# Performance work log

Hardware: AMD Instinct MI355X
Metric: run time of the kernel (lower is better)

Reference implementation:

```python
import jax, jax.numpy as jnp
import numpy as np
import math

B, T, D = 4, 4096, 256


def setup_inputs() -> dict:
    key = jax.random.key(0)
    ks = jax.random.split(key, 12)
    stdv = 1.0 / math.sqrt(D)
    u = lambda k, shape, s: jax.random.uniform(k, shape, jnp.float32, -s, s)
    return {
        "query": jax.random.normal(ks[0], (B, T, D), jnp.float32),
        "value": jax.random.normal(ks[1], (B, T, D), jnp.float32),
        # gate vectors, init uniform(-1/sqrt(D), 1/sqrt(D)) per reset_parameters
        "q_vec": u(ks[2], (D,), stdv),
        "k_vec": u(ks[3], (D,), stdv),
        "v_vec": u(ks[4], (D,), stdv),
        # nn.Linear params (torch default init: uniform(-1/sqrt(fan_in), ...))
        "Wq": u(ks[5], (D, D), stdv), "bq": u(ks[6], (D,), stdv),
        "Ws": u(ks[7], (D, D), stdv), "bs": u(ks[8], (D,), stdv),
        "Wt": u(ks[9], (D, D), stdv), "bt": u(ks[10], (D,), stdv),
    }


def reference(query, value, q_vec, k_vec, v_vec, Wq, bq, Ws, bs, Wt, bt):
    d = query.shape[-1]
    # q = Linear(query) * sigmoid(query_vector)
    q = (jnp.einsum('btd,ed->bte', query, Wq) + bq) * jax.nn.sigmoid(q_vec)
    # k = value * sigmoid(key_vector)
    k = value * jax.nn.sigmoid(k_vec)
    # v gate: infer=False branch -> GLU-style gate of sigmoid(value_vector)
    vv = jax.nn.sigmoid(v_vec)
    v_gate = jax.nn.sigmoid(Ws @ vv + bs) * jnp.tanh(Wt @ vv + bt)
    v = value * v_gate
    # scores [B, T, T]
    w = jnp.einsum('bqd,bkd->bqk', q, k) / jnp.sqrt(jnp.float32(d))
    # causal: multiply by tril mask then replace exact zeros with -inf
    # (faithful to the original's weight[weight==0]=-inf quirk)
    Tn = w.shape[-1]
    tril = jnp.tril(jnp.ones((Tn, Tn), w.dtype))
    w = w * tril
    w = jnp.where(w == 0.0, -jnp.inf, w)
    attn = jax.nn.softmax(w, axis=-1)
    return jnp.einsum('bqk,bkd->bqd', attn, v)
```

## Files before the change

kernel.cpp:

```cpp
#include <hip/hip_runtime.h>
#include <math.h>

#define D 256
#define T 4096
#define KT (17408/2)
#define VT (20480/2)
#define PSTR ((size_t)4*T*D)

typedef __attribute__((ext_vector_type(8))) short bf16x8;
typedef __attribute__((ext_vector_type(4))) float f32x4;
typedef __attribute__((ext_vector_type(4))) unsigned short u16x4;

__device__ __forceinline__ unsigned short f2bf(float x){
  unsigned int u = __float_as_uint(x);
  unsigned int r = (u + 0x7FFFu + ((u >> 16) & 1u)) >> 16;
  return (unsigned short)r;
}
__device__ __forceinline__ float bf2f(unsigned short h){
  return __uint_as_float(((unsigned int)h) << 16);
}

__device__ __forceinline__ void gl_lds16(const void* g, void* l){
  __builtin_amdgcn_global_load_lds((const __attribute__((address_space(1))) unsigned int*)g,
                                   (__attribute__((address_space(3))) unsigned int*)l, 16, 0, 0);
}

__global__ __launch_bounds__(256) void prep_kernel(
    const float* __restrict__ q_vec, const float* __restrict__ k_vec,
    const float* __restrict__ v_vec, const float* __restrict__ Ws,
    const float* __restrict__ bs, const float* __restrict__ Wt,
    const float* __restrict__ bt, const float* __restrict__ Wq,
    float* __restrict__ gates, unsigned short* __restrict__ wq_g){
  int t = threadIdx.x;
  if(blockIdx.x == 0){
    __shared__ float vv[D];
    vv[t]         = 1.f/(1.f + __expf(-v_vec[t]));
    gates[t]      = 1.f/(1.f + __expf(-q_vec[t]));
    gates[D + t]  = 1.f/(1.f + __expf(-k_vec[t]));
    __syncthreads();
    const f32x4* wsr = (const f32x4*)(Ws + (size_t)t*D);
    const f32x4* wtr = (const f32x4*)(Wt + (size_t)t*D);
    const f32x4* vvv = (const f32x4*)vv;
    f32x4 a0 = {0,0,0,0}, a1 = {0,0,0,0}, c0 = {0,0,0,0}, c1 = {0,0,0,0};
    for(int i=0;i<64;i+=2){
      f32x4 v0 = vvv[i], v1 = vvv[i+1];
      a0 += wsr[i]*v0; a1 += wsr[i+1]*v1;
      c0 += wtr[i]*v0; c1 += wtr[i+1]*v1;
    }
    f32x4 as = a0 + a1, cs = c0 + c1;
    float s1 = bs[t] + as[0]+as[1]+as[2]+as[3];
    float s2 = bt[t] + cs[0]+cs[1]+cs[2]+cs[3];
    gates[2*D + t] = (1.f/(1.f + __expf(-s1))) * tanhf(s2);
  } else {
    int kc = blockIdx.x - 1;
    const float* src = Wq + (size_t)t*D + kc*32;
    unsigned short* dst = wq_g + (size_t)kc*10240 + t*40;
    #pragma unroll
    for(int u=0;u<4;u++){
      bf16x8 pk;
      #pragma unroll
      for(int x=0;x<8;x++) pk[x] = (short)f2bf(src[u*8+x]);
      *(bf16x8*)&dst[u*8] = pk;
    }
  }
}

__global__ __launch_bounds__(256) void mid_kernel(
    const float* __restrict__ query, const unsigned short* __restrict__ wq_g,
    const float* __restrict__ bq, const float* __restrict__ gates,
    unsigned short* __restrict__ q_g,
    const float* __restrict__ value,
    unsigned short* __restrict__ k_g, unsigned short* __restrict__ vt_g){
  __shared__ __align__(16) unsigned short smem[2][10240];
  int tid = threadIdx.x;
  if(blockIdx.x < 256){
    int w = tid >> 6; int l = tid & 63;
    int lr = l & 15, lc = l >> 4;
    int r0 = blockIdx.x * 64;
    f32x4 acc[16];
    #pragma unroll
    for(int n=0;n<16;n++) acc[n] = (f32x4){0.f,0.f,0.f,0.f};
    const float* qrow = query + (size_t)(r0 + w*16 + lr)*D;
    #pragma unroll
    for(int i=0;i<5;i++){ int c = i*256 + tid; gl_lds16(wq_g + c*8, (char*)smem[0] + c*16); }
    __syncthreads();
    int cur = 0;
    for(int kc=0; kc<8; kc++){
      if(kc < 7){
        #pragma unroll
        for(int i=0;i<5;i++){ int c = i*256 + tid;
          gl_lds16(wq_g + (size_t)(kc+1)*10240 + c*8, (char*)smem[cur^1] + c*16); }
      }
      bf16x8 af;
      {
        const float* s = qrow + kc*32 + lc*8;
        #pragma unroll
        for(int x=0;x<8;x++) af[x] = (short)f2bf(s[x]);
      }
      #pragma unroll
      for(int n=0;n<16;n++){
        bf16x8 bfrag = *(const bf16x8*)&smem[cur][(n*16 + lr)*40 + lc*8];
        acc[n] = __builtin_amdgcn_mfma_f32_16x16x32_bf16(af, bfrag, acc[n], 0, 0, 0);
      }
      __syncthreads();
      cur ^= 1;
    }
    #pragma unroll
    for(int n=0;n<16;n++){
      int col = n*16 + lr;
      float bb = bq[col], gg = gates[col];
      #pragma unroll
      for(int r=0;r<4;r++){
        int row = r0 + w*16 + lc*4 + r;
        q_g[(size_t)row*D + col] = f2bf((acc[n][r] + bb) * gg);
      }
    }
  } else {
    int bid2 = blockIdx.x - 256;
    int b = bid2 >> 7, jt = bid2 & 127;
    const float* vbase = value + ((size_t)b*T + jt*32)*D;
    const float* gk = gates + D;
    const float* vg = gates + 2*D;
    unsigned short* kt = k_g  + (size_t)bid2 * KT;
    unsigned short* vt = vt_g + (size_t)bid2 * VT;
    #pragma unroll
    for(int i=0;i<4;i++){
      int g = i*256 + tid; int j = g >> 5, c = g & 31;
      const float* src = vbase + j*D + c*8;
      bf16x8 pk;
      #pragma unroll
      for(int x=0;x<8;x++) pk[x] = (short)f2bf(src[x] * gk[c*8+x]);
      *(bf16x8*)&kt[j*264 + c*8] = pk;
    }
    float* lds = (float*)smem;
    for(int c=0;c<4;c++){
      __syncthreads();
      {
        int row = tid >> 3, cg = tid & 7;
        const float* src = vbase + (size_t)row*D + c*64 + cg*8;
        f32x4 v0 = *(const f32x4*)src;
        f32x4 v1 = *(const f32x4*)(src + 4);
        *(f32x4*)&lds[row*68 + cg*8]     = v0;
        *(f32x4*)&lds[row*68 + cg*8 + 4] = v1;
      }
      __syncthreads();
      {
        int d0l = tid >> 2, u = tid & 3;
        int d0 = c*64 + d0l;
        float gd = vg[d0];
        bf16x8 pk;
        #pragma unroll
        for(int x=0;x<8;x++){
          int p = u*8 + x;
          int ksrc = ((p>>3)<<2) + (p&3) + (((p>>2)&1)<<4);
          pk[x] = (short)f2bf(lds[ksrc*68 + d0l] * gd);
        }
        *(bf16x8*)&vt[d0*40 + u*8] = pk;
      }
    }
  }
}

__global__ __launch_bounds__(512, 4) void flash_kernel(
    const unsigned short* __restrict__ q_g,
    const unsigned short* __restrict__ k_g,
    const unsigned short* __restrict__ vt_g,
    unsigned short* __restrict__ parts,
    float* __restrict__ ml, int logS){
  __shared__ __align__(16) unsigned short kbuf[2][KT];
  __shared__ __align__(16) unsigned short vbuf[2][VT];
  int tid = threadIdx.x; int w = tid >> 6, l = tid & 63;
  int lr = l & 15, lc = l >> 4;
  int S = 1 << logS;
  int bid = blockIdx.x;
  int x = bid & 7; int b = x >> 1; int p = x & 1;
  int item = bid >> 3;
  int half = S >> 1;
  int rblk = 31 - (item / half);
  int s = p*half + (item & (half - 1));
  int r0 = rblk * 128;
  int wrow0 = r0 + w*16;
  int nt = 4*rblk + 4;
  int jt0 = (s*nt) >> logS, jt1 = ((s+1)*nt) >> logS;
  int gr = wrow0 + lr;

  bf16x8 qf[8];
  {
    const unsigned short* qbase = q_g + ((size_t)b*T + wrow0 + lr)*D + lc*8;
    #pragma unroll
    for(int kc=0;kc<8;kc++) qf[kc] = *(const bf16x8*)(qbase + kc*32);
  }
  f32x4 o[16];
  #pragma unroll
  for(int n=0;n<16;n++) o[n] = (f32x4){0.f,0.f,0.f,0.f};
  float m = -INFINITY, lsum = 0.f;

  const unsigned short* ktb = k_g  + (size_t)b*128*KT;
  const unsigned short* vtb = vt_g + (size_t)b*128*VT;

  if(jt1 > jt0){
    const unsigned short* ks = ktb + (size_t)jt0*KT;
    const unsigned short* vs = vtb + (size_t)jt0*VT;
    for(int c=w; c<37; c+=8){
      if(c < 17) gl_lds16(ks + c*512 + l*8, (char*)kbuf[jt0&1] + c*1024);
      else       gl_lds16(vs + (c-17)*512 + l*8, (char*)vbuf[jt0&1] + (c-17)*1024);
    }
  }

  for(int jt=jt0; jt<jt1; jt++){
    int cur = jt & 1;
    asm volatile("s_waitcnt vmcnt(0)" ::: "memory");
    __builtin_amdgcn_s_barrier();
    __builtin_amdgcn_sched_barrier(0);
    if(jt+1 < jt1){
      const unsigned short* ks = ktb + (size_t)(jt+1)*KT;
      const unsigned short* vs = vtb + (size_t)(jt+1)*VT;
      for(int c=w; c<37; c+=8){
        if(c < 17) gl_lds16(ks + c*512 + l*8, (char*)kbuf[cur^1] + c*1024);
        else       gl_lds16(vs + (c-17)*512 + l*8, (char*)vbuf[cur^1] + (c-17)*1024);
      }
    }
    int j0 = jt*32;
    bool active = (j0 <= wrow0 + 15);
    if(active){
      f32x4 s0a = {0,0,0,0}, s0b = {0,0,0,0}, s1a = {0,0,0,0}, s1b = {0,0,0,0};
      #pragma unroll
      for(int kc=0;kc<4;kc++){
        bf16x8 k0 = *(const bf16x8*)&kbuf[cur][lr*264        + (kc*4 + lc)*8];
        bf16x8 k1 = *(const bf16x8*)&kbuf[cur][(16 + lr)*264 + (kc*4 + lc)*8];
        bf16x8 k0h = *(const bf16x8*)&kbuf[cur][lr*264        + ((kc+4)*4 + lc)*8];
        bf16x8 k1h = *(const bf16x8*)&kbuf[cur][(16 + lr)*264 + ((kc+4)*4 + lc)*8];
        s0a = __builtin_amdgcn_mfma_f32_16x16x32_bf16(k0,  qf[kc],   s0a, 0,0,0);
        s1a = __builtin_amdgcn_mfma_f32_16x16x32_bf16(k1,  qf[kc],   s1a, 0,0,0);
        s0b = __builtin_amdgcn_mfma_f32_16x16x32_bf16(k0h, qf[kc+4], s0b, 0,0,0);
        s1b = __builtin_amdgcn_mfma_f32_16x16x32_bf16(k1h, qf[kc+4], s1b, 0,0,0);
      }
      f32x4 s0 = s0a + s0b, s1 = s1a + s1b;
      float sv0[4], sv1[4];
      #pragma unroll
      for(int r=0;r<4;r++){
        float x0 = s0[r]*0.0625f; int gj0 = j0 + lc*4 + r;
        float x1 = s1[r]*0.0625f; int gj1 = gj0 + 16;
        if(gj0 > gr || x0 == 0.0f) x0 = -INFINITY;
        if(gj1 > gr || x1 == 0.0f) x1 = -INFINITY;
        sv0[r]=x0; sv1[r]=x1;
      }
      float pmax = fmaxf(fmaxf(fmaxf(sv0[0],sv0[1]),fmaxf(sv0[2],sv0[3])),
                         fmaxf(fmaxf(sv1[0],sv1[1]),fmaxf(sv1[2],sv1[3])));
      pmax = fmaxf(pmax, __shfl_xor(pmax, 16));
      pmax = fmaxf(pmax, __shfl_xor(pmax, 32));
      bool mv = (pmax > m + 8.0f);
      float mn = mv ? pmax : m;
      float alpha = mv ? __expf(m - mn) : 1.0f;
      float p0[4], p1[4];
      #pragma unroll
      for(int r=0;r<4;r++){
        p0[r] = (sv0[r] == -INFINITY) ? 0.f : __expf(sv0[r] - mn);
        p1[r] = (sv1[r] == -INFINITY) ? 0.f : __expf(sv1[r] - mn);
      }
      unsigned long long anymv = __builtin_amdgcn_ballot_w64(mv);
      if(anymv){
        float a0 = __shfl(alpha, lc*4 + 0);
        float a1 = __shfl(alpha, lc*4 + 1);
        float a2 = __shfl(alpha, lc*4 + 2);
        float a3 = __shfl(alpha, lc*4 + 3);
        #pragma unroll
        for(int n=0;n<16;n++){
          o[n][0] *= a0; o[n][1] *= a1; o[n][2] *= a2; o[n][3] *= a3;
        }
      }
      float ps = ((p0[0]+p0[1])+(p0[2]+p0[3])) + ((p1[0]+p1[1])+(p1[2]+p1[3]));
      lsum = lsum*alpha + ps;
      m = mn;
      bf16x8 pa;
      #pragma unroll
      for(int r=0;r<4;r++){ pa[r] = (short)f2bf(p0[r]); pa[4+r] = (short)f2bf(p1[r]); }
      #pragma unroll
      for(int n=0;n<16;n++){
        bf16x8 vf = *(const bf16x8*)&vbuf[cur][(n*16 + lr)*40 + lc*8];
        o[n] = __builtin_amdgcn_mfma_f32_16x16x32_bf16(pa, vf, o[n], 0,0,0);
      }
    }
  }

  unsigned short* obase = parts + (size_t)s*PSTR + ((size_t)b*T + wrow0)*D;
  #pragma unroll
  for(int r=0;r<4;r++){
    #pragma unroll
    for(int n=0;n<16;n++){
      obase[(size_t)(lc*4 + r)*D + n*16 + lr] = f2bf(o[n][r]);
    }
  }
  lsum += __shfl_xor(lsum, 16);
  lsum += __shfl_xor(lsum, 32);
  if(l < 16){
    float* mlb = ml + ((size_t)s*4*T + (size_t)b*T + wrow0 + lr)*2;
    mlb[0] = m; mlb[1] = lsum;
  }
}

__global__ __launch_bounds__(256) void combine_kernel(
    const unsigned short* __restrict__ parts, const float* __restrict__ ml,
    float* __restrict__ out, int S){
  size_t idx = (size_t)blockIdx.x*256 + threadIdx.x;
  size_t e = idx*4;
  size_t row = e >> 8;
  float msv[8], lsv[8];
  float mm = -INFINITY;
  for(int s=0;s<S;s++){
    msv[s] = ml[((size_t)s*4*T + row)*2];
    lsv[s] = ml[((size_t)s*4*T + row)*2 + 1];
    mm = fmaxf(mm, msv[s]);
  }
  float denom = 0.f;
  f32x4 acc = {0.f,0.f,0.f,0.f};
  for(int s=0;s<S;s++){
    float as = __expf(msv[s] - mm);
    if(as != 0.0f){
      denom += as*lsv[s];
      u16x4 v = *(const u16x4*)&parts[(size_t)s*PSTR + e];
      #pragma unroll
      for(int xx=0;xx<4;xx++) acc[xx] += as*bf2f(v[xx]);
    }
  }
  float inv = 1.0f/denom;
  f32x4 r;
  #pragma unroll
  for(int xx=0;xx<4;xx++) r[xx] = acc[xx]*inv;
  *(f32x4*)&out[e] = r;
}

extern "C" void kernel_launch(void* const* d_in, const int* in_sizes, int n_in,
                              void* d_out, int out_size, void* d_ws, size_t ws_size,
                              hipStream_t stream){
  (void)in_sizes; (void)n_in; (void)out_size;
  const float* query = (const float*)d_in[0];
  const float* value = (const float*)d_in[1];
  const float* q_vec = (const float*)d_in[2];
  const float* k_vec = (const float*)d_in[3];
  const float* v_vec = (const float*)d_in[4];
  const float* Wq    = (const float*)d_in[5];
  const float* bq    = (const float*)d_in[6];
  const float* Ws    = (const float*)d_in[7];
  const float* bs    = (const float*)d_in[8];
  const float* Wt    = (const float*)d_in[9];
  const float* bt    = (const float*)d_in[10];
  char* ws = (char*)d_ws;
  unsigned short* q_g  = (unsigned short*)(ws);
  unsigned short* k_g  = (unsigned short*)(ws + 8388608);
  unsigned short* vt_g = (unsigned short*)(ws + 17301504);
  unsigned short* wq_g = (unsigned short*)(ws + 27787264);
  float* gates         = (float*)(ws + 27951104);
  unsigned short* parts= (unsigned short*)(ws + 27955200);
  float* out = (float*)d_out;

  size_t base = 27955200;
  size_t mlsz = (size_t)8*4*T*2*4;
  int logS;
  if(ws_size >= base + 8*PSTR*2 + mlsz)      logS = 3;
  else if(ws_size >= base + 4*PSTR*2 + mlsz) logS = 2;
  else                                       logS = 1;
  int S = 1 << logS;
  float* ml = (float*)(ws + base + (size_t)S*PSTR*2);

  hipLaunchKernelGGL(prep_kernel, dim3(9),   dim3(256), 0, stream,
                     q_vec, k_vec, v_vec, Ws, bs, Wt, bt, Wq, gates, wq_g);
  hipLaunchKernelGGL(mid_kernel,  dim3(768), dim3(256), 0, stream,
                     query, wq_g, bq, gates, q_g, value, k_g, vt_g);
  hipLaunchKernelGGL(flash_kernel, dim3(128*S), dim3(512), 0, stream,
                     q_g, k_g, vt_g, parts, ml, logS);
  hipLaunchKernelGGL(combine_kernel, dim3((4*T*D/4)/256), dim3(256), 0, stream,
                     parts, ml, out, S);
}
```

Baseline: 134.3 us.

## Give each wave two 16-row query tiles and halve flash block size

Flash blocks shrink from 512 to 256 threads. Each wave now owns 32 query rows as two 16-row tiles, so every K and V fragment read from LDS feeds two MFMAs, which cuts LDS traffic per FLOP. The causal mask comparison now runs only on the diagonal tile, and the explicit -inf check before exp is dropped. In exchange, doubled accumulators and Q fragments raise register pressure and lower the waves per block, and fewer waves share each cooperative K/V load.

Measured after the change: 119.9 us. -10.7%, faster.

```diff
diff --git a/kernel.cpp b/kernel.cpp
--- a/kernel.cpp
+++ b/kernel.cpp
@@ -161,7 +161,7 @@
   }
 }
 
-__global__ __launch_bounds__(512, 4) void flash_kernel(
+__global__ __launch_bounds__(256, 2) void flash_kernel(
     const unsigned short* __restrict__ q_g,
     const unsigned short* __restrict__ k_g,
     const unsigned short* __restrict__ vt_g,
@@ -177,23 +177,30 @@
   int item = bid >> 3;
   int half = S >> 1;
   int rblk = 31 - (item / half);
-  int s = p*half + (item & (half - 1));
+  int s = p*half + (item % half);
   int r0 = rblk * 128;
-  int wrow0 = r0 + w*16;
+  int wrow0 = r0 + w*32;
   int nt = 4*rblk + 4;
   int jt0 = (s*nt) >> logS, jt1 = ((s+1)*nt) >> logS;
-  int gr = wrow0 + lr;
-
-  bf16x8 qf[8];
+  int grA = wrow0 + lr;
+  int grB = wrow0 + 16 + lr;
+  int diagA = (wrow0 + 15) >> 5;
+  int diagB = (wrow0 + 31) >> 5;
+
+  bf16x8 qfA[8], qfB[8];
   {
-    const unsigned short* qbase = q_g + ((size_t)b*T + wrow0 + lr)*D + lc*8;
-    #pragma unroll
-    for(int kc=0;kc<8;kc++) qf[kc] = *(const bf16x8*)(qbase + kc*32);
-  }
-  f32x4 o[16];
+    const unsigned short* qa = q_g + ((size_t)b*T + grA)*D + lc*8;
+    const unsigned short* qb = q_g + ((size_t)b*T + grB)*D + lc*8;
+    #pragma unroll
+    for(int kc=0;kc<8;kc++){
+      qfA[kc] = *(const bf16x8*)(qa + kc*32);
+      qfB[kc] = *(const bf16x8*)(qb + kc*32);
+    }
+  }
+  f32x4 oA[16], oB[16];
   #pragma unroll
-  for(int n=0;n<16;n++) o[n] = (f32x4){0.f,0.f,0.f,0.f};
-  float m = -INFINITY, lsum = 0.f;
+  for(int n=0;n<16;n++){ oA[n] = (f32x4){0.f,0.f,0.f,0.f}; oB[n] = (f32x4){0.f,0.f,0.f,0.f}; }
+  float mA = -INFINITY, lsA = 0.f, mB = -INFINITY, lsB = 0.f;
 
   const unsigned short* ktb = k_g  + (size_t)b*128*KT;
   const unsigned short* vtb = vt_g + (size_t)b*128*VT;
@@ -201,7 +208,7 @@
   if(jt1 > jt0){
     const unsigned short* ks = ktb + (size_t)jt0*KT;
     const unsigned short* vs = vtb + (size_t)jt0*VT;
-    for(int c=w; c<37; c+=8){
+    for(int c=w; c<37; c+=4){
       if(c < 17) gl_lds16(ks + c*512 + l*8, (char*)kbuf[jt0&1] + c*1024);
       else       gl_lds16(vs + (c-17)*512 + l*8, (char*)vbuf[jt0&1] + (c-17)*1024);
     }
@@ -215,87 +222,166 @@
     if(jt+1 < jt1){
       const unsigned short* ks = ktb + (size_t)(jt+1)*KT;
       const unsigned short* vs = vtb + (size_t)(jt+1)*VT;
-      for(int c=w; c<37; c+=8){
+      for(int c=w; c<37; c+=4){
         if(c < 17) gl_lds16(ks + c*512 + l*8, (char*)kbuf[cur^1] + c*1024);
         else       gl_lds16(vs + (c-17)*512 + l*8, (char*)vbuf[cur^1] + (c-17)*1024);
       }
     }
     int j0 = jt*32;
-    bool active = (j0 <= wrow0 + 15);
-    if(active){
-      f32x4 s0a = {0,0,0,0}, s0b = {0,0,0,0}, s1a = {0,0,0,0}, s1b = {0,0,0,0};
-      #pragma unroll
-      for(int kc=0;kc<4;kc++){
-        bf16x8 k0 = *(const bf16x8*)&kbuf[cur][lr*264        + (kc*4 + lc)*8];
-        bf16x8 k1 = *(const bf16x8*)&kbuf[cur][(16 + lr)*264 + (kc*4 + lc)*8];
-        bf16x8 k0h = *(const bf16x8*)&kbuf[cur][lr*264        + ((kc+4)*4 + lc)*8];
-        bf16x8 k1h = *(const bf16x8*)&kbuf[cur][(16 + lr)*264 + ((kc+4)*4 + lc)*8];
-        s0a = __builtin_amdgcn_mfma_f32_16x16x32_bf16(k0,  qf[kc],   s0a, 0,0,0);
-        s1a = __builtin_amdgcn_mfma_f32_16x16x32_bf16(k1,  qf[kc],   s1a, 0,0,0);
-        s0b = __builtin_amdgcn_mfma_f32_16x16x32_bf16(k0h, qf[kc+4], s0b, 0,0,0);
-        s1b = __builtin_amdgcn_mfma_f32_16x16x32_bf16(k1h, qf[kc+4], s1b, 0,0,0);
-      }
-      f32x4 s0 = s0a + s0b, s1 = s1a + s1b;
-      float sv0[4], sv1[4];
-      #pragma unroll
-      for(int r=0;r<4;r++){
-        float x0 = s0[r]*0.0625f; int gj0 = j0 + lc*4 + r;
-        float x1 = s1[r]*0.0625f; int gj1 = gj0 + 16;
-        if(gj0 > gr || x0 == 0.0f) x0 = -INFINITY;
-        if(gj1 > gr || x1 == 0.0f) x1 = -INFINITY;
-        sv0[r]=x0; sv1[r]=x1;
-      }
-      float pmax = fmaxf(fmaxf(fmaxf(sv0[0],sv0[1]),fmaxf(sv0[2],sv0[3])),
-                         fmaxf(fmaxf(sv1[0],sv1[1]),fmaxf(sv1[2],sv1[3])));
-      pmax = fmaxf(pmax, __shfl_xor(pmax, 16));
-      pmax = fmaxf(pmax, __shfl_xor(pmax, 32));
-      bool mv = (pmax > m + 8.0f);
-      float mn = mv ? pmax : m;
-      float alpha = mv ? __expf(m - mn) : 1.0f;
-      float p0[4], p1[4];
-      #pragma unroll
-      for(int r=0;r<4;r++){
-        p0[r] = (sv0[r] == -INFINITY) ? 0.f : __expf(sv0[r] - mn);
-        p1[r] = (sv1[r] == -INFINITY) ? 0.f : __expf(sv1[r] - mn);
-      }
-      unsigned long long anymv = __builtin_amdgcn_ballot_w64(mv);
-      if(anymv){
-        float a0 = __shfl(alpha, lc*4 + 0);
-        float a1 = __shfl(alpha, lc*4 + 1);
-        float a2 = __shfl(alpha, lc*4 + 2);
-        float a3 = __shfl(alpha, lc*4 + 3);
+    bool actA = (j0 <= wrow0 + 15);
+    bool actB = (j0 <= wrow0 + 31);
+    if(actB){
+      f32x4 sA0={0,0,0,0}, sA1={0,0,0,0}, sB0={0,0,0,0}, sB1={0,0,0,0};
+      if(actA){
+        #pragma unroll
+        for(int kc=0;kc<8;kc++){
+          bf16x8 k0 = *(const bf16x8*)&kbuf[cur][lr*264        + (kc*4 + lc)*8];
+          bf16x8 k1 = *(const bf16x8*)&kbuf[cur][(16 + lr)*264 + (kc*4 + lc)*8];
+          sA0 = __builtin_amdgcn_mfma_f32_16x16x32_bf16(k0, qfA[kc], sA0, 0,0,0);
+          sA1 = __builtin_amdgcn_mfma_f32_16x16x32_bf16(k1, qfA[kc], sA1, 0,0,0);
+          sB0 = __builtin_amdgcn_mfma_f32_16x16x32_bf16(k0, qfB[kc], sB0, 0,0,0);
+          sB1 = __builtin_amdgcn_mfma_f32_16x16x32_bf16(k1, qfB[kc], sB1, 0,0,0);
+        }
+      } else {
+        #pragma unroll
+        for(int kc=0;kc<8;kc++){
+          bf16x8 k0 = *(const bf16x8*)&kbuf[cur][lr*264        + (kc*4 + lc)*8];
+          bf16x8 k1 = *(const bf16x8*)&kbuf[cur][(16 + lr)*264 + (kc*4 + lc)*8];
+          sB0 = __builtin_amdgcn_mfma_f32_16x16x32_bf16(k0, qfB[kc], sB0, 0,0,0);
+          sB1 = __builtin_amdgcn_mfma_f32_16x16x32_bf16(k1, qfB[kc], sB1, 0,0,0);
+        }
+      }
+      bf16x8 paA, paB;
+      if(actA){
+        float sv0[4], sv1[4];
+        if(jt == diagA){
+          #pragma unroll
+          for(int r=0;r<4;r++){
+            float x0 = sA0[r]*0.0625f; int gj0 = j0 + lc*4 + r;
+            float x1 = sA1[r]*0.0625f; int gj1 = gj0 + 16;
+            sv0[r] = (gj0 > grA || x0 == 0.0f) ? -INFINITY : x0;
+            sv1[r] = (gj1 > grA || x1 == 0.0f) ? -INFINITY : x1;
+          }
+        } else {
+          #pragma unroll
+          for(int r=0;r<4;r++){
+            float x0 = sA0[r]*0.0625f;
+            float x1 = sA1[r]*0.0625f;
+            sv0[r] = (x0 == 0.0f) ? -INFINITY : x0;
+            sv1[r] = (x1 == 0.0f) ? -INFINITY : x1;
+          }
+        }
+        float pmax = fmaxf(fmaxf(fmaxf(sv0[0],sv0[1]),fmaxf(sv0[2],sv0[3])),
+                           fmaxf(fmaxf(sv1[0],sv1[1]),fmaxf(sv1[2],sv1[3])));
+        pmax = fmaxf(pmax, __shfl_xor(pmax, 16));
+        pmax = fmaxf(pmax, __shfl_xor(pmax, 32));
+        bool mv = (pmax > mA + 8.0f);
+        float mn = mv ? pmax : mA;
+        float alpha = mv ? __expf(mA - mn) : 1.0f;
+        float p0[4], p1[4];
+        #pragma unroll
+        for(int r=0;r<4;r++){
+          p0[r] = __expf(sv0[r] - mn);
+          p1[r] = __expf(sv1[r] - mn);
+        }
+        if(__builtin_amdgcn_ballot_w64(mv)){
+          float a0 = __shfl(alpha, lc*4 + 0);
+          float a1 = __shfl(alpha, lc*4 + 1);
+          float a2 = __shfl(alpha, lc*4 + 2);
+          float a3 = __shfl(alpha, lc*4 + 3);
+          #pragma unroll
+          for(int n=0;n<16;n++){
+            oA[n][0] *= a0; oA[n][1] *= a1; oA[n][2] *= a2; oA[n][3] *= a3;
+          }
+        }
+        float ps = ((p0[0]+p0[1])+(p0[2]+p0[3])) + ((p1[0]+p1[1])+(p1[2]+p1[3]));
+        lsA = lsA*alpha + ps;
+        mA = mn;
+        #pragma unroll
+        for(int r=0;r<4;r++){ paA[r] = (short)f2bf(p0[r]); paA[4+r] = (short)f2bf(p1[r]); }
+      }
+      {
+        float sv0[4], sv1[4];
+        if(jt == diagB){
+          #pragma unroll
+          for(int r=0;r<4;r++){
+            float x0 = sB0[r]*0.0625f; int gj0 = j0 + lc*4 + r;
+            float x1 = sB1[r]*0.0625f; int gj1 = gj0 + 16;
+            sv0[r] = (gj0 > grB || x0 == 0.0f) ? -INFINITY : x0;
+            sv1[r] = (gj1 > grB || x1 == 0.0f) ? -INFINITY : x1;
+          }
+        } else {
+          #pragma unroll
+          for(int r=0;r<4;r++){
+            float x0 = sB0[r]*0.0625f;
+            float x1 = sB1[r]*0.0625f;
+            sv0[r] = (x0 == 0.0f) ? -INFINITY : x0;
+            sv1[r] = (x1 == 0.0f) ? -INFINITY : x1;
+          }
+        }
+        float pmax = fmaxf(fmaxf(fmaxf(sv0[0],sv0[1]),fmaxf(sv0[2],sv0[3])),
+                           fmaxf(fmaxf(sv1[0],sv1[1]),fmaxf(sv1[2],sv1[3])));
+        pmax = fmaxf(pmax, __shfl_xor(pmax, 16));
+        pmax = fmaxf(pmax, __shfl_xor(pmax, 32));
+        bool mv = (pmax > mB + 8.0f);
+        float mn = mv ? pmax : mB;
+        float alpha = mv ? __expf(mB - mn) : 1.0f;
+        float p0[4], p1[4];
+        #pragma unroll
+        for(int r=0;r<4;r++){
+          p0[r] = __expf(sv0[r] - mn);
+          p1[r] = __expf(sv1[r] - mn);
+        }
+        if(__builtin_amdgcn_ballot_w64(mv)){
+          float a0 = __shfl(alpha, lc*4 + 0);
+          float a1 = __shfl(alpha, lc*4 + 1);
+          float a2 = __shfl(alpha, lc*4 + 2);
+          float a3 = __shfl(alpha, lc*4 + 3);
+          #pragma unroll
+          for(int n=0;n<16;n++){
+            oB[n][0] *= a0; oB[n][1] *= a1; oB[n][2] *= a2; oB[n][3] *= a3;
+          }
+        }
+        float ps = ((p0[0]+p0[1])+(p0[2]+p0[3])) + ((p1[0]+p1[1])+(p1[2]+p1[3]));
+        lsB = lsB*alpha + ps;
+        mB = mn;
+        #pragma unroll
+        for(int r=0;r<4;r++){ paB[r] = (short)f2bf(p0[r]); paB[4+r] = (short)f2bf(p1[r]); }
+      }
+      if(actA){
         #pragma unroll
         for(int n=0;n<16;n++){
-          o[n][0] *= a0; o[n][1] *= a1; o[n][2] *= a2; o[n][3] *= a3;
-        }
-      }
-      float ps = ((p0[0]+p0[1])+(p0[2]+p0[3])) + ((p1[0]+p1[1])+(p1[2]+p1[3]));
-      lsum = lsum*alpha + ps;
-      m = mn;
-      bf16x8 pa;
-      #pragma unroll
-      for(int r=0;r<4;r++){ pa[r] = (short)f2bf(p0[r]); pa[4+r] = (short)f2bf(p1[r]); }
-      #pragma unroll
-      for(int n=0;n<16;n++){
-        bf16x8 vf = *(const bf16x8*)&vbuf[cur][(n*16 + lr)*40 + lc*8];
-        o[n] = __builtin_amdgcn_mfma_f32_16x16x32_bf16(pa, vf, o[n], 0,0,0);
-      }
-    }
-  }
-
-  unsigned short* obase = parts + (size_t)s*PSTR + ((size_t)b*T + wrow0)*D;
+          bf16x8 vf = *(const bf16x8*)&vbuf[cur][(n*16 + lr)*40 + lc*8];
+          oA[n] = __builtin_amdgcn_mfma_f32_16x16x32_bf16(paA, vf, oA[n], 0,0,0);
+          oB[n] = __builtin_amdgcn_mfma_f32_16x16x32_bf16(paB, vf, oB[n], 0,0,0);
+        }
+      } else {
+        #pragma unroll
+        for(int n=0;n<16;n++){
+          bf16x8 vf = *(const bf16x8*)&vbuf[cur][(n*16 + lr)*40 + lc*8];
+          oB[n] = __builtin_amdgcn_mfma_f32_16x16x32_bf16(paB, vf, oB[n], 0,0,0);
+        }
+      }
+    }
+  }
+
+  unsigned short* obaseA = parts + (size_t)s*PSTR + ((size_t)b*T + wrow0)*D;
+  unsigned short* obaseB = obaseA + (size_t)16*D;
   #pragma unroll
   for(int r=0;r<4;r++){
     #pragma unroll
     for(int n=0;n<16;n++){
-      obase[(size_t)(lc*4 + r)*D + n*16 + lr] = f2bf(o[n][r]);
-    }
-  }
-  lsum += __shfl_xor(lsum, 16);
-  lsum += __shfl_xor(lsum, 32);
+      obaseA[(size_t)(lc*4 + r)*D + n*16 + lr] = f2bf(oA[n][r]);
+      obaseB[(size_t)(lc*4 + r)*D + n*16 + lr] = f2bf(oB[n][r]);
+    }
+  }
+  lsA += __shfl_xor(lsA, 16); lsA += __shfl_xor(lsA, 32);
+  lsB += __shfl_xor(lsB, 16); lsB += __shfl_xor(lsB, 32);
   if(l < 16){
-    float* mlb = ml + ((size_t)s*4*T + (size_t)b*T + wrow0 + lr)*2;
-    mlb[0] = m; mlb[1] = lsum;
+    float* mlbA = ml + ((size_t)s*4*T + (size_t)b*T + wrow0 + lr)*2;
+    mlbA[0] = mA; mlbA[1] = lsA;
+    float* mlbB = ml + ((size_t)s*4*T + (size_t)b*T + wrow0 + 16 + lr)*2;
+    mlbB[0] = mB; mlbB[1] = lsB;
   }
 }
 
@@ -367,7 +453,7 @@
                      q_vec, k_vec, v_vec, Ws, bs, Wt, bt, Wq, gates, wq_g);
   hipLaunchKernelGGL(mid_kernel,  dim3(768), dim3(256), 0, stream,
                      query, wq_g, bq, gates, q_g, value, k_g, vt_g);
-  hipLaunchKernelGGL(flash_kernel, dim3(128*S), dim3(512), 0, stream,
+  hipLaunchKernelGGL(flash_kernel, dim3(128*S), dim3(256), 0, stream,
                      q_g, k_g, vt_g, parts, ml, logS);
   hipLaunchKernelGGL(combine_kernel, dim3((4*T*D/4)/256), dim3(256), 0, stream,
                      parts, ml, out, S);
```
